# Kernel optimization log

Hardware: AMD Instinct MI355X
Metric: run time of the kernel (lower is better)

## Reference

```python
import jax, jax.numpy as jnp
import numpy as np

N, E, C, K, M = 16384, 512, 128, 2048, 4
H1, H2 = 128, 256
EPS = 1e-5


def setup_inputs() -> dict:
    key = jax.random.key(0)
    ks = jax.random.split(key, 32)
    r = lambda k, shape, s=0.02: jax.random.normal(k, shape, dtype=jnp.float32) * s
    inp = {
        'x': jax.random.normal(ks[0], (N, E), dtype=jnp.float32),
        # per-book encoder params, stacked over M
        'enc_W1': r(ks[1], (M, E, H1)), 'enc_b1': r(ks[2], (M, H1)),
        'bn1_g': 1.0 + r(ks[3], (M, H1)), 'bn1_b': r(ks[4], (M, H1)),
        'bn1_m': r(ks[5], (M, H1), 0.1), 'bn1_v': jnp.ones((M, H1), jnp.float32),
        'enc_W2': r(ks[6], (M, H1, H2)), 'enc_b2': r(ks[7], (M, H2)),
        'bn2_g': 1.0 + r(ks[8], (M, H2)), 'bn2_b': r(ks[9], (M, H2)),
        'bn2_m': r(ks[10], (M, H2), 0.1), 'bn2_v': jnp.ones((M, H2), jnp.float32),
        'enc_W3': r(ks[11], (M, H2, C)), 'enc_b3': r(ks[12], (M, C)),
        # codebooks init uniform(-1/K, 1/K) as in torch source
        'codebooks': jax.random.uniform(ks[13], (M, K, C), jnp.float32, -1.0 / K, 1.0 / K),
        # decoder params
        'dec_W1': r(ks[14], (C, H2)), 'dec_b1': r(ks[15], (H2,)),
        'dbn1_g': 1.0 + r(ks[16], (H2,)), 'dbn1_b': r(ks[17], (H2,)),
        'dbn1_m': r(ks[18], (H2,), 0.1), 'dbn1_v': jnp.ones((H2,), jnp.float32),
        'dec_W2': r(ks[19], (H2, H1)), 'dec_b2': r(ks[20], (H1,)),
        'dbn2_g': 1.0 + r(ks[21], (H1,)), 'dbn2_b': r(ks[22], (H1,)),
        'dbn2_m': r(ks[23], (H1,), 0.1), 'dbn2_v': jnp.ones((H1,), jnp.float32),
        'dec_W3': r(ks[24], (H1, E)), 'dec_b3': r(ks[25], (E,)),
    }
    return inp


def _bn(h, g, b, m, v):
    # eval-mode BatchNorm1d with running stats (dropout inactive in eval)
    return (h - m) * (g / jnp.sqrt(v + EPS)) + b


def reference(x, enc_W1, enc_b1, bn1_g, bn1_b, bn1_m, bn1_v,
              enc_W2, enc_b2, bn2_g, bn2_b, bn2_m, bn2_v,
              enc_W3, enc_b3, codebooks,
              dec_W1, dec_b1, dbn1_g, dbn1_b, dbn1_m, dbn1_v,
              dec_W2, dec_b2, dbn2_g, dbn2_b, dbn2_m, dbn2_v,
              dec_W3, dec_b3):
    # encoders for all M books at once: [M, N, *]
    h = jnp.einsum('ne,mef->mnf', x, enc_W1) + enc_b1[:, None, :]
    h = jax.nn.relu(_bn(h, bn1_g[:, None], bn1_b[:, None], bn1_m[:, None], bn1_v[:, None]))
    h = jnp.einsum('mnf,mfg->mng', h, enc_W2) + enc_b2[:, None, :]
    h = jax.nn.relu(_bn(h, bn2_g[:, None], bn2_b[:, None], bn2_m[:, None], bn2_v[:, None]))
    ze = jnp.einsum('mng,mgc->mnc', h, enc_W3) + enc_b3[:, None, :]  # [M,N,C]

    # squared-distance VQ via dot-product expansion (same math as broadcast cdist)
    ze_sq = jnp.sum(ze * ze, axis=-1)                     # [M,N]
    cb_sq = jnp.sum(codebooks * codebooks, axis=-1)       # [M,K]
    cross = jnp.einsum('mnc,mkc->mnk', ze, codebooks)     # [M,N,K]
    dist = ze_sq[..., None] + cb_sq[:, None, :] - 2.0 * cross
    idx = jnp.argmin(dist, axis=-1)                       # [M,N]
    ce = jnp.take_along_axis(codebooks, idx[:, :, None], axis=1)  # [M,N,C]

    zq = jnp.sum(ce, axis=0)                              # [N,C]

    d = jnp.matmul(zq, dec_W1) + dec_b1
    d = jax.nn.relu(_bn(d, dbn1_g, dbn1_b, dbn1_m, dbn1_v))
    d = jnp.matmul(d, dec_W2) + dec_b2
    d = jax.nn.relu(_bn(d, dbn2_g, dbn2_b, dbn2_m, dbn2_v))
    x_hat = jnp.matmul(d, dec_W3) + dec_b3

    # res_list / ce_list returned as stacked [M,N,C] arrays
    return (x_hat, ze, ce)
```

## Files before the change

kernel.cpp:

```cpp
#include <hip/hip_runtime.h>
#include <hip/hip_bf16.h>
#include <stdint.h>

#define N_ROWS 16384
#define E_DIM 512
#define C_DIM 128
#define K_CODES 2048
#define M_BOOKS 4
#define H1_DIM 128
#define H2_DIM 256
#define EPS_V 1e-5f

typedef __attribute__((ext_vector_type(8))) short short8v;
typedef __attribute__((ext_vector_type(4))) float f32x4;

#if defined(__has_builtin)
#if __has_builtin(__builtin_amdgcn_global_load_lds)
#define HAVE_GLL 1
#endif
#endif

#ifdef HAVE_GLL
__device__ __forceinline__ void gll16(const void* g, void* l) {
    __builtin_amdgcn_global_load_lds(
        (const __attribute__((address_space(1))) uint32_t*)g,
        (__attribute__((address_space(3))) uint32_t*)l, 16, 0, 0);
}
#endif

__device__ __forceinline__ unsigned int mapmono(float d) {
    unsigned int ub = __float_as_uint(d);
    return (ub & 0x80000000u) ? ~ub : (ub | 0x80000000u);
}
__device__ __forceinline__ float unmapmono(unsigned int u) {
    unsigned int bits = (u & 0x80000000u) ? (u & 0x7FFFFFFFu) : ~u;
    return __uint_as_float(bits);
}

template<int BK, bool BNRELU>
__global__ __launch_bounds__(256, 4) void gemm128(
    const float* __restrict__ A, const float* __restrict__ B,
    const float* __restrict__ bias, const float* __restrict__ bn_g,
    const float* __restrict__ bn_b, const float* __restrict__ bn_m,
    const float* __restrict__ bn_v, float* __restrict__ C,
    int Kd, int Hc, size_t sA, size_t sB, size_t sP, size_t sC)
{
    __shared__ float As[BK][128];
    __shared__ float Bs[BK][128];
    const int z = blockIdx.z;
    A += (size_t)z * sA; B += (size_t)z * sB; bias += (size_t)z * sP;
    if (BNRELU) {
        bn_g += (size_t)z * sP; bn_b += (size_t)z * sP;
        bn_m += (size_t)z * sP; bn_v += (size_t)z * sP;
    }
    const int t = threadIdx.x;
    const int tx = t & 15, ty = t >> 4;
    const int row0 = blockIdx.y * 128, col0 = blockIdx.x * 128;
    const int ar = t & 127, ak = (t >> 7) * 4;
    const int bc = (t & 31) * 4, bk0 = t >> 5;

    float acc[8][8] = {};
    for (int k0 = 0; k0 < Kd; k0 += BK) {
        #pragma unroll
        for (int l = 0; l < BK / 8; ++l) {
            const int lk = ak + l * 8;
            float4 av = *(const float4*)(A + (size_t)(row0 + ar) * Kd + (k0 + lk));
            As[lk+0][ar] = av.x; As[lk+1][ar] = av.y;
            As[lk+2][ar] = av.z; As[lk+3][ar] = av.w;
            const int kb = bk0 + l * 8;
            *(float4*)&Bs[kb][bc] =
                *(const float4*)(B + (size_t)(k0 + kb) * Hc + (col0 + bc));
        }
        __syncthreads();
        #pragma unroll
        for (int kk = 0; kk < BK; ++kk) {
            float a[8], b[8];
            *(float4*)&a[0] = *(const float4*)&As[kk][ty*4];
            *(float4*)&a[4] = *(const float4*)&As[kk][64 + ty*4];
            *(float4*)&b[0] = *(const float4*)&Bs[kk][tx*4];
            *(float4*)&b[4] = *(const float4*)&Bs[kk][64 + tx*4];
            #pragma unroll
            for (int i = 0; i < 8; ++i)
                #pragma unroll
                for (int j = 0; j < 8; ++j)
                    acc[i][j] = fmaf(a[i], b[j], acc[i][j]);
        }
        __syncthreads();
    }
    float bi[8], sc[8], mu[8], be[8];
    #pragma unroll
    for (int j = 0; j < 8; ++j) {
        const int col = col0 + ((j < 4) ? (tx*4 + j) : (64 + tx*4 + j - 4));
        bi[j] = bias[col];
        if (BNRELU) {
            sc[j] = bn_g[col] / sqrtf(bn_v[col] + EPS_V);
            mu[j] = bn_m[col]; be[j] = bn_b[col];
        }
    }
    #pragma unroll
    for (int i = 0; i < 8; ++i) {
        const int row = row0 + ((i < 4) ? (ty*4 + i) : (64 + ty*4 + i - 4));
        float v[8];
        #pragma unroll
        for (int j = 0; j < 8; ++j) {
            v[j] = acc[i][j] + bi[j];
            if (BNRELU) {
                float p = (v[j] - mu[j]) * sc[j];
                asm volatile("" : "+v"(p));
                v[j] = fmaxf(p + be[j], 0.0f);
            }
        }
        float* cp = C + (size_t)z * sC + (size_t)row * Hc + col0;
        *(float4*)(cp + tx*4)      = *(const float4*)&v[0];
        *(float4*)(cp + 64 + tx*4) = *(const float4*)&v[4];
    }
}

__global__ __launch_bounds__(256) void rowsq_np(const float* __restrict__ X,
                                                float* __restrict__ out, int rows)
{
    const int r = blockIdx.x * blockDim.x + threadIdx.x;
    if (r >= rows) return;
    const float* p = X + (size_t)r * C_DIM;
    float rr[8];
    #pragma unroll
    for (int j = 0; j < 8; ++j) {
        float v = p[j]; float s2 = v * v;
        asm volatile("" : "+v"(s2));
        rr[j] = s2;
    }
    for (int i = 8; i < C_DIM; i += 8) {
        #pragma unroll
        for (int j = 0; j < 8; ++j) {
            float v = p[i + j]; float s2 = v * v;
            asm volatile("" : "+v"(s2));
            rr[j] = rr[j] + s2;
        }
    }
    out[r] = ((rr[0]+rr[1]) + (rr[2]+rr[3])) + ((rr[4]+rr[5]) + (rr[6]+rr[7]));
}

__global__ __launch_bounds__(256) void split_ze(
    const float* __restrict__ ze, uint16_t* __restrict__ zeAf,
    float* __restrict__ zs, float* __restrict__ eps)
{
    const int m = blockIdx.y;
    const int r = blockIdx.x * 256 + threadIdx.x;
    const size_t g = (size_t)m * N_ROWS + r;
    const float* p = ze + g * C_DIM;
    float a[C_DIM];
    #pragma unroll
    for (int c4 = 0; c4 < C_DIM/4; ++c4) {
        float4 v = *(const float4*)(p + c4*4);
        a[c4*4+0]=v.x; a[c4*4+1]=v.y; a[c4*4+2]=v.z; a[c4*4+3]=v.w;
    }
    {
        float rr[8];
        #pragma unroll
        for (int j = 0; j < 8; ++j) {
            float v = a[j]; float s2 = v*v; asm volatile("" : "+v"(s2)); rr[j]=s2;
        }
        #pragma unroll
        for (int i = 8; i < C_DIM; i += 8)
            #pragma unroll
            for (int j = 0; j < 8; ++j) {
                float v = a[i+j]; float s2 = v*v; asm volatile("" : "+v"(s2));
                rr[j] = rr[j] + s2;
            }
        zs[g] = ((rr[0]+rr[1]) + (rr[2]+rr[3])) + ((rr[4]+rr[5]) + (rr[6]+rr[7]));
    }
    {
        float sab = 0.0f;
        #pragma unroll
        for (int c = 0; c < C_DIM; ++c) sab += fabsf(a[c]);
        eps[g] = sab * 4.8828125e-4f * 1e-4f + 1e-9f;
    }
    const int rt = r >> 7, rl = r & 127;
    uint16_t* base = zeAf + (size_t)m * 4194304 + ((size_t)rt * 4096 + rl) * 8;
    #pragma unroll
    for (int k8 = 0; k8 < 32; ++k8) {
        uint16_t u[8];
        #pragma unroll
        for (int j = 0; j < 8; ++j) {
            const int c = ((k8 < 16) ? k8 : (k8 - 16)) * 8 + j;
            __hip_bfloat16 h = __float2bfloat16(a[c]);
            if (k8 >= 16) {
                float res = a[c] - __bfloat162float(h);
                h = __float2bfloat16(res);
            }
            u[j] = *(uint16_t*)&h;
        }
        *(float4*)(base + (size_t)k8 * 1024) = *(const float4*)u;
    }
}

__global__ __launch_bounds__(256) void split_cb(
    const float* __restrict__ cb, uint16_t* __restrict__ cbBf,
    float* __restrict__ cbsq, int* __restrict__ count)
{
    const int m = blockIdx.z;
    const int k = blockIdx.x * 256 + threadIdx.x;
    if (m == 0 && k == 0) *count = 0;
    const float* p = cb + ((size_t)m * K_CODES + k) * C_DIM;
    float a[C_DIM];
    #pragma unroll
    for (int c4 = 0; c4 < C_DIM/4; ++c4) {
        float4 v = *(const float4*)(p + c4*4);
        a[c4*4+0]=v.x; a[c4*4+1]=v.y; a[c4*4+2]=v.z; a[c4*4+3]=v.w;
    }
    {
        float rr[8];
        #pragma unroll
        for (int j = 0; j < 8; ++j) {
            float v = a[j]; float s2 = v*v; asm volatile("" : "+v"(s2)); rr[j]=s2;
        }
        #pragma unroll
        for (int i = 8; i < C_DIM; i += 8)
            #pragma unroll
            for (int j = 0; j < 8; ++j) {
                float v = a[i+j]; float s2 = v*v; asm volatile("" : "+v"(s2));
                rr[j] = rr[j] + s2;
            }
        cbsq[(size_t)m * K_CODES + k] =
            ((rr[0]+rr[1]) + (rr[2]+rr[3])) + ((rr[4]+rr[5]) + (rr[6]+rr[7]));
    }
    const int ct = k >> 7, kl = k & 127;
    uint16_t* base = cbBf + (((size_t)m * 16 + ct) * 4096 + kl) * 8;
    #pragma unroll
    for (int k8 = 0; k8 < 32; ++k8) {
        uint16_t u[8];
        #pragma unroll
        for (int j = 0; j < 8; ++j) {
            const int c = ((k8 < 16) ? k8 : (k8 - 16)) * 8 + j;
            __hip_bfloat16 h = __float2bfloat16(a[c]);
            if (k8 >= 16) {
                float res = a[c] - __bfloat162float(h);
                h = __float2bfloat16(res);
            }
            u[j] = *(uint16_t*)&h;
        }
        *(float4*)(base + (size_t)k8 * 1024) = *(const float4*)u;
    }
}

__global__ __launch_bounds__(256, 3) void vq_mfma(
    const uint16_t* __restrict__ zeAf, const uint16_t* __restrict__ cbBf,
    const float* __restrict__ zs, const float* __restrict__ cbsq,
    unsigned long long* __restrict__ keysB, unsigned long long* __restrict__ keysS)
{
    __shared__ __align__(16) uint16_t BhS[2][4096], BlS[2][4096];
    __shared__ unsigned long long kb2[128][2];

    const int t = threadIdx.x;
    const int l = t & 63, w = t >> 6;
    const int ct = blockIdx.x, rt = blockIdx.y, m = blockIdx.z;
    const int lq = l >> 4, lc = l & 15;

    const uint16_t* Ag = zeAf + (size_t)m * 4194304 + (size_t)rt * 32768;
    const uint16_t* Bg = cbBf + ((size_t)m * 16 + ct) * 32768;

#ifdef HAVE_GLL
    {
        const uint16_t* sBh = Bg;
        const uint16_t* sBl = Bg + (size_t)16 * 1024;
        gll16(sBh + t*8,        BhS[0] + t*8);
        gll16(sBh + 2048 + t*8, BhS[0] + 2048 + t*8);
        gll16(sBl + t*8,        BlS[0] + t*8);
        gll16(sBl + 2048 + t*8, BlS[0] + 2048 + t*8);
    }
    __syncthreads();
#else
    float4 rh0, rh1, rl0, rl1;
    {
        const uint16_t* sBh = Bg;
        const uint16_t* sBl = Bg + (size_t)16 * 1024;
        rh0 = *(const float4*)(sBh + t*8);
        rh1 = *(const float4*)(sBh + 2048 + t*8);
        rl0 = *(const float4*)(sBl + t*8);
        rl1 = *(const float4*)(sBl + 2048 + t*8);
    }
    *(float4*)(BhS[0] + t*8)        = rh0;
    *(float4*)(BhS[0] + 2048 + t*8) = rh1;
    *(float4*)(BlS[0] + t*8)        = rl0;
    *(float4*)(BlS[0] + 2048 + t*8) = rl1;
    __syncthreads();
#endif

    f32x4 acc[2][8] = {};
    #pragma unroll
    for (int s = 0; s < 4; ++s) {
        const int cur = s & 1;
        if (s < 3) {
            const uint16_t* sBh = Bg + (size_t)((s+1)*4) * 1024;
            const uint16_t* sBl = Bg + (size_t)(16 + (s+1)*4) * 1024;
#ifdef HAVE_GLL
            gll16(sBh + t*8,        BhS[cur^1] + t*8);
            gll16(sBh + 2048 + t*8, BhS[cur^1] + 2048 + t*8);
            gll16(sBl + t*8,        BlS[cur^1] + t*8);
            gll16(sBl + 2048 + t*8, BlS[cur^1] + 2048 + t*8);
#else
            rh0 = *(const float4*)(sBh + t*8);
            rh1 = *(const float4*)(sBh + 2048 + t*8);
            rl0 = *(const float4*)(sBl + t*8);
            rl1 = *(const float4*)(sBl + 2048 + t*8);
#endif
        }
        short8v zeh[2], zel[2], cbf[8];
        #pragma unroll
        for (int rc = 0; rc < 2; ++rc) {
            const int row = w*32 + rc*16 + lc;
            zeh[rc] = *(const short8v*)(Ag + ((size_t)(s*4 + lq)*128 + row)*8);
            zel[rc] = *(const short8v*)(Ag + ((size_t)(16 + s*4 + lq)*128 + row)*8);
        }
        #pragma unroll
        for (int c8 = 0; c8 < 8; ++c8)
            cbf[c8] = *(const short8v*)(BhS[cur] + ((size_t)lq*128 + c8*16 + lc)*8);
        #pragma unroll
        for (int rc = 0; rc < 2; ++rc)
            #pragma unroll
            for (int c8 = 0; c8 < 8; ++c8)
                acc[rc][c8] = __builtin_amdgcn_mfma_f32_16x16x32_bf16(
                    cbf[c8], zeh[rc], acc[rc][c8], 0, 0, 0);
        #pragma unroll
        for (int rc = 0; rc < 2; ++rc)
            #pragma unroll
            for (int c8 = 0; c8 < 8; ++c8)
                acc[rc][c8] = __builtin_amdgcn_mfma_f32_16x16x32_bf16(
                    cbf[c8], zel[rc], acc[rc][c8], 0, 0, 0);
        #pragma unroll
        for (int c8 = 0; c8 < 8; ++c8)
            cbf[c8] = *(const short8v*)(BlS[cur] + ((size_t)lq*128 + c8*16 + lc)*8);
        #pragma unroll
        for (int rc = 0; rc < 2; ++rc)
            #pragma unroll
            for (int c8 = 0; c8 < 8; ++c8)
                acc[rc][c8] = __builtin_amdgcn_mfma_f32_16x16x32_bf16(
                    cbf[c8], zeh[rc], acc[rc][c8], 0, 0, 0);
#ifndef HAVE_GLL
        if (s < 3) {
            *(float4*)(BhS[cur^1] + t*8)        = rh0;
            *(float4*)(BhS[cur^1] + 2048 + t*8) = rh1;
            *(float4*)(BlS[cur^1] + t*8)        = rl0;
            *(float4*)(BlS[cur^1] + 2048 + t*8) = rl1;
        }
#endif
        __syncthreads();
    }

    const float* csb = cbsq + (size_t)m * K_CODES + ct*128;
    #pragma unroll
    for (int rc = 0; rc < 2; ++rc) {
        const int row = w*32 + rc*16 + lc;
        float bd = 3.4e38f, sd = 3.4e38f;
        int bidx = 0;
        #pragma unroll
        for (int c8 = 0; c8 < 8; ++c8)
            #pragma unroll
            for (int q = 0; q < 4; ++q) {
                const int cl = c8*16 + lq*4 + q;
                const float d = fmaf(-2.0f, acc[rc][c8][q], csb[cl]);
                const float mx = fmaxf(bd, d);
                sd = fminf(sd, mx);
                if (d < bd) { bd = d; bidx = ct*128 + cl; }
            }
        #pragma unroll
        for (int mk = 16; mk < 64; mk <<= 1) {
            const float ob = __shfl_xor(bd, mk);
            const int   oi = __shfl_xor(bidx, mk);
            const float os = __shfl_xor(sd, mk);
            const float mx = fmaxf(bd, ob);
            sd = fminf(fminf(sd, os), mx);
            if (ob < bd) { bd = ob; bidx = oi; }
        }
        if (lq == 0) {
            kb2[row][0] = ((unsigned long long)mapmono(bd) << 32) | (unsigned)bidx;
            kb2[row][1] = ((unsigned long long)mapmono(sd) << 32) | 0xFFFFFFFFu;
        }
    }
    __syncthreads();
    if (t < 128) {
        const unsigned long long b = kb2[t][0];
        const unsigned long long s2v = kb2[t][1];
        const size_t g = (size_t)m * N_ROWS + rt*128 + t;
        const unsigned long long old = atomicMin(&keysB[g], b);
        const unsigned long long disp = (b < old) ? old : b;
        const unsigned long long cand = (s2v < disp) ? s2v : disp;
        atomicMin(&keysS[g], cand);
    }
}

__global__ __launch_bounds__(256) void vq_flag(
    const float* __restrict__ ze, const float* __restrict__ cb,
    const float* __restrict__ zs, const float* __restrict__ cbsq,
    const unsigned long long* __restrict__ keysB,
    const unsigned long long* __restrict__ keysS,
    const float* __restrict__ eps, int* __restrict__ list, int* __restrict__ count)
{
    const int m = blockIdx.y;
    const int r = blockIdx.x * 256 + threadIdx.x;
    const size_t g = (size_t)m * N_ROWS + r;
    const unsigned long long kbv = keysB[g];
    const int code = (int)(kbv & 0xFFFFFFFFull);
    const float db = unmapmono((unsigned int)(kbv >> 32));
    const float ds2 = unmapmono((unsigned int)(keysS[g] >> 32));
    const float* zr = ze + g * C_DIM;
    const float* cr = cb + ((size_t)m * K_CODES + code) * C_DIM;
    float acc = 0.0f;
    #pragma unroll
    for (int c = 0; c < C_DIM; ++c) acc = fmaf(zr[c], cr[c], acc);
    const float dex = fmaf(-2.0f, acc, cbsq[(size_t)m * K_CODES + code]);
    const float e = eps[g];
    if ((ds2 - db <= 2.0f * e) || (fabsf(dex - db) > e)) {
        const int p = atomicAdd(count, 1);
        list[p] = (int)g;
    }
}

__global__ __launch_bounds__(256) void vq_cleanup2(
    const float* __restrict__ ze, const float* __restrict__ cb,
    const float* __restrict__ zs, const float* __restrict__ cbsq,
    const int* __restrict__ list, const int* __restrict__ count,
    unsigned long long* __restrict__ keysB)
{
    __shared__ float zrow[C_DIM];
    __shared__ unsigned long long red[4];
    const int t = threadIdx.x;
    const int w = t >> 6, l = t & 63;
    const int nflag = *count;
    for (int idx = blockIdx.x; idx < nflag; idx += gridDim.x) {
        const int g = list[idx];
        const int m = g >> 14;
        if (t < 32)
            *(float4*)(zrow + t*4) = *(const float4*)(ze + (size_t)g * C_DIM + t*4);
        __syncthreads();
        const float zsr = zs[g];
        const int k0 = t * 8;
        const float* cbp = cb + ((size_t)m * K_CODES + k0) * C_DIM;
        const float* csp = cbsq + (size_t)m * K_CODES + k0;
        float acc8[8] = {};
        for (int c4 = 0; c4 < C_DIM/4; ++c4) {
            const float4 a4 = *(const float4*)(zrow + c4*4);
            #pragma unroll
            for (int u = 0; u < 8; ++u) {
                const float4 b4 = *(const float4*)(cbp + (size_t)u * C_DIM + c4*4);
                acc8[u] = fmaf(a4.x, b4.x, acc8[u]);
                acc8[u] = fmaf(a4.y, b4.y, acc8[u]);
                acc8[u] = fmaf(a4.z, b4.z, acc8[u]);
                acc8[u] = fmaf(a4.w, b4.w, acc8[u]);
            }
        }
        unsigned long long bk = ~0ull;
        #pragma unroll
        for (int u = 0; u < 8; ++u) {
            const float tmp = zsr + csp[u];
            float m2a = 2.0f * acc8[u];
            asm volatile("" : "+v"(m2a));
            const float d = tmp - m2a;
            const unsigned long long key =
                ((unsigned long long)mapmono(d) << 32) | (unsigned)(k0 + u);
            bk = (key < bk) ? key : bk;
        }
        #pragma unroll
        for (int off2 = 32; off2 > 0; off2 >>= 1) {
            const unsigned long long o = __shfl_down(bk, off2);
            bk = (o < bk) ? o : bk;
        }
        if (l == 0) red[w] = bk;
        __syncthreads();
        if (t == 0) {
            unsigned long long b = red[0];
            b = (red[1] < b) ? red[1] : b;
            b = (red[2] < b) ? red[2] : b;
            b = (red[3] < b) ? red[3] : b;
            keysB[g] = b;
        }
        __syncthreads();
    }
}

__global__ __launch_bounds__(256) void split_wB(
    const float* __restrict__ W, uint16_t* __restrict__ Wf, int Kd, int Hc)
{
    const int z = blockIdx.z;
    W += (size_t)z * Kd * Hc;
    Wf += (size_t)z * Kd * Hc * 2;
    const int ct = blockIdx.x, k8 = blockIdx.y;
    const int Sh = Kd / 8, S = Kd / 4;
    const int t = threadIdx.x;
    #pragma unroll
    for (int e0 = 0; e0 < 2; ++e0) {
        const int e = t + e0 * 256;
        const int h = e >> 3, j = e & 7;
        const float v = W[(size_t)(k8*8 + j) * Hc + ct*64 + h];
        __hip_bfloat16 hi = __float2bfloat16(v);
        float res = v - __bfloat162float(hi);
        __hip_bfloat16 lo = __float2bfloat16(res);
        Wf[(((size_t)ct*S + k8)*64 + h)*8 + j]      = *(uint16_t*)&hi;
        Wf[(((size_t)ct*S + Sh + k8)*64 + h)*8 + j] = *(uint16_t*)&lo;
    }
}

template<bool BNRELU>
__global__ __launch_bounds__(256, 3) void mfma_fused(
    const float* __restrict__ A, const uint16_t* __restrict__ Wf,
    const float* __restrict__ bias, const float* __restrict__ bn_g,
    const float* __restrict__ bn_b, const float* __restrict__ bn_m,
    const float* __restrict__ bn_v, float* __restrict__ C, int Kd, int Hc,
    size_t sA, size_t sWf, size_t sP, size_t sC)
{
    __shared__ __align__(16) uint16_t Ah[4096], Al[4096], Bh[2048], Bl[2048];
    const int z = blockIdx.z;
    A += (size_t)z * sA; Wf += (size_t)z * sWf; bias += (size_t)z * sP;
    if (BNRELU) {
        bn_g += (size_t)z * sP; bn_b += (size_t)z * sP;
        bn_m += (size_t)z * sP; bn_v += (size_t)z * sP;
    }
    C += (size_t)z * sC;

    const int t = threadIdx.x;
    const int l = t & 63, w = t >> 6;
    const int kq = l >> 4, lc = l & 15;
    const int row0 = blockIdx.y * 128, col0 = blockIdx.x * 64;
    const int Sh = Kd / 8, S = Kd / 4;
    const uint16_t* Wct = Wf + (size_t)blockIdx.x * S * 512;

    f32x4 acc[2][4] = {};
    const int arow = t & 127, khalf = t >> 7;
    for (int ks = 0; ks < Kd / 32; ++ks) {
        const float* ap = A + (size_t)(row0 + arow) * Kd + ks*32 + khalf*16;
        float fa[16];
        *(float4*)&fa[0]  = *(const float4*)(ap);
        *(float4*)&fa[4]  = *(const float4*)(ap + 4);
        *(float4*)&fa[8]  = *(const float4*)(ap + 8);
        *(float4*)&fa[12] = *(const float4*)(ap + 12);
        uint16_t ah[16], al16[16];
        #pragma unroll
        for (int i = 0; i < 16; ++i) {
            __hip_bfloat16 h = __float2bfloat16(fa[i]);
            float res = fa[i] - __bfloat162float(h);
            __hip_bfloat16 lo = __float2bfloat16(res);
            ah[i] = *(uint16_t*)&h; al16[i] = *(uint16_t*)&lo;
        }
        #pragma unroll
        for (int kql = 0; kql < 2; ++kql) {
            const int kq_ = khalf*2 + kql;
            *(float4*)(Ah + ((size_t)kq_*128 + arow)*8) = *(const float4*)&ah[kql*8];
            *(float4*)(Al + ((size_t)kq_*128 + arow)*8) = *(const float4*)&al16[kql*8];
        }
        {
            const int sec = t >> 6, off = (t & 63) * 8;
            *(float4*)(Bh + (size_t)sec*512 + off) =
                *(const float4*)(Wct + ((size_t)(ks*4 + sec))*512 + off);
            *(float4*)(Bl + (size_t)sec*512 + off) =
                *(const float4*)(Wct + ((size_t)(Sh + ks*4 + sec))*512 + off);
        }
        __syncthreads();
        short8v afh[2], afl[2], bfh[4], bfl[4];
        #pragma unroll
        for (int r2 = 0; r2 < 2; ++r2) {
            afh[r2] = *(const short8v*)(Ah + ((size_t)kq*128 + w*32 + r2*16 + lc)*8);
            afl[r2] = *(const short8v*)(Al + ((size_t)kq*128 + w*32 + r2*16 + lc)*8);
        }
        #pragma unroll
        for (int c4 = 0; c4 < 4; ++c4) {
            bfh[c4] = *(const short8v*)(Bh + ((size_t)kq*64 + c4*16 + lc)*8);
            bfl[c4] = *(const short8v*)(Bl + ((size_t)kq*64 + c4*16 + lc)*8);
        }
        #pragma unroll
        for (int r2 = 0; r2 < 2; ++r2)
            #pragma unroll
            for (int c4 = 0; c4 < 4; ++c4) {
                acc[r2][c4] = __builtin_amdgcn_mfma_f32_16x16x32_bf16(
                    afh[r2], bfh[c4], acc[r2][c4], 0, 0, 0);
                acc[r2][c4] = __builtin_amdgcn_mfma_f32_16x16x32_bf16(
                    afl[r2], bfh[c4], acc[r2][c4], 0, 0, 0);
                acc[r2][c4] = __builtin_amdgcn_mfma_f32_16x16x32_bf16(
                    afh[r2], bfl[c4], acc[r2][c4], 0, 0, 0);
            }
        __syncthreads();
    }
    #pragma unroll
    for (int c4 = 0; c4 < 4; ++c4) {
        const int col = col0 + c4*16 + lc;
        const float bi = bias[col];
        float sc = 0.f, mu = 0.f, be = 0.f;
        if (BNRELU) {
            sc = bn_g[col] / sqrtf(bn_v[col] + EPS_V);
            mu = bn_m[col]; be = bn_b[col];
        }
        #pragma unroll
        for (int r2 = 0; r2 < 2; ++r2)
            #pragma unroll
            for (int q = 0; q < 4; ++q) {
                const int row = row0 + w*32 + r2*16 + kq*4 + q;
                float v = acc[r2][c4][q] + bi;
                if (BNRELU) v = fmaxf((v - mu) * sc + be, 0.0f);
                C[(size_t)row * Hc + col] = v;
            }
    }
}

__global__ __launch_bounds__(256, 4) void vq_argmin(
    const float* __restrict__ ze, const float* __restrict__ cb,
    const float* __restrict__ ze_sq, const float* __restrict__ cb_sq,
    unsigned long long* __restrict__ keys)
{
    __shared__ __align__(16) char smem_raw[32768];
    float* As = (float*)smem_raw;
    float* Bs = As + 32*128;
    unsigned long long* kb = (unsigned long long*)smem_raw;
    const int m = blockIdx.z;
    const float* Zm  = ze + (size_t)m * N_ROWS * C_DIM;
    const float* Bm  = cb + (size_t)m * K_CODES * C_DIM;
    const float* zsm = ze_sq + (size_t)m * N_ROWS;
    const float* csm = cb_sq + (size_t)m * K_CODES;
    const int t = threadIdx.x;
    const int tx = t & 15, ty = t >> 4;
    const int row0 = blockIdx.y * 128, col0 = blockIdx.x * 128;
    const int ar = t & 127, ak = (t >> 7) * 4;
    float acc[8][8] = {};
    for (int k0 = 0; k0 < C_DIM; k0 += 32) {
        #pragma unroll
        for (int l = 0; l < 4; ++l) {
            const int lk = ak + l * 8;
            float4 av = *(const float4*)(Zm + (size_t)(row0 + ar) * C_DIM + (k0 + lk));
            As[(lk+0)*128+ar] = av.x; As[(lk+1)*128+ar] = av.y;
            As[(lk+2)*128+ar] = av.z; As[(lk+3)*128+ar] = av.w;
            float4 bv = *(const float4*)(Bm + (size_t)(col0 + ar) * C_DIM + (k0 + lk));
            Bs[(lk+0)*128+ar] = bv.x; Bs[(lk+1)*128+ar] = bv.y;
            Bs[(lk+2)*128+ar] = bv.z; Bs[(lk+3)*128+ar] = bv.w;
        }
        __syncthreads();
        #pragma unroll
        for (int kk = 0; kk < 32; ++kk) {
            float a[8], b[8];
            *(float4*)&a[0] = *(const float4*)&As[kk*128 + ty*4];
            *(float4*)&a[4] = *(const float4*)&As[kk*128 + 64 + ty*4];
            *(float4*)&b[0] = *(const float4*)&Bs[kk*128 + tx*4];
            *(float4*)&b[4] = *(const float4*)&Bs[kk*128 + 64 + tx*4];
            #pragma unroll
            for (int i = 0; i < 8; ++i)
                #pragma unroll
                for (int j = 0; j < 8; ++j)
                    acc[i][j] = fmaf(a[i], b[j], acc[i][j]);
        }
        __syncthreads();
    }
    unsigned long long mykey[8];
    #pragma unroll
    for (int i = 0; i < 8; ++i) {
        const int rloc = (i < 4) ? (ty*4 + i) : (64 + ty*4 + i - 4);
        const float zsv = zsm[row0 + rloc];
        unsigned long long bk = ~0ull;
        #pragma unroll
        for (int j = 0; j < 8; ++j) {
            const int code = col0 + ((j < 4) ? (tx*4 + j) : (64 + tx*4 + j - 4));
            const float d = (zsv + csm[code]) - 2.0f * acc[i][j];
            const unsigned long long key =
                ((unsigned long long)mapmono(d) << 32) | (unsigned)code;
            bk = (key < bk) ? key : bk;
        }
        mykey[i] = bk;
    }
    __syncthreads();
    #pragma unroll
    for (int i = 0; i < 8; ++i) {
        const int rloc = (i < 4) ? (ty*4 + i) : (64 + ty*4 + i - 4);
        kb[rloc*17 + tx] = mykey[i];
    }
    __syncthreads();
    if (t < 128) {
        unsigned long long bk = kb[t*17];
        #pragma unroll
        for (int k2 = 1; k2 < 16; ++k2) {
            const unsigned long long k = kb[t*17 + k2];
            bk = (k < bk) ? k : bk;
        }
        atomicMin(&keys[(size_t)m * N_ROWS + row0 + t], bk);
    }
}

__global__ __launch_bounds__(256) void gather_ce_zq(
    const unsigned long long* __restrict__ keys, const float* __restrict__ cb,
    float* __restrict__ ce_out, float* __restrict__ zq)
{
    const int gid = blockIdx.x * 256 + threadIdx.x;
    const int n = gid >> 7, c = gid & 127;
    float s = 0.0f;
    #pragma unroll
    for (int m = 0; m < M_BOOKS; ++m) {
        const int idx = (int)(keys[(size_t)m * N_ROWS + n] & 0xFFFFFFFFull);
        const float v = cb[((size_t)m * K_CODES + idx) * C_DIM + c];
        ce_out[((size_t)m * N_ROWS + n) * (size_t)C_DIM + c] = v;
        s += v;
    }
    zq[gid] = s;
}

extern "C" void kernel_launch(void* const* d_in, const int* in_sizes, int n_in,
                              void* d_out, int out_size, void* d_ws, size_t ws_size,
                              hipStream_t stream)
{
    const float* x   = (const float*)d_in[0];
    const float* eW1 = (const float*)d_in[1];
    const float* eb1 = (const float*)d_in[2];
    const float* g1  = (const float*)d_in[3];
    const float* b1  = (const float*)d_in[4];
    const float* m1  = (const float*)d_in[5];
    const float* v1  = (const float*)d_in[6];
    const float* eW2 = (const float*)d_in[7];
    const float* eb2 = (const float*)d_in[8];
    const float* g2  = (const float*)d_in[9];
    const float* b2  = (const float*)d_in[10];
    const float* m2  = (const float*)d_in[11];
    const float* v2  = (const float*)d_in[12];
    const float* eW3 = (const float*)d_in[13];
    const float* eb3 = (const float*)d_in[14];
    const float* cb  = (const float*)d_in[15];
    const float* dW1 = (const float*)d_in[16];
    const float* db1 = (const float*)d_in[17];
    const float* dg1 = (const float*)d_in[18];
    const float* dbb1= (const float*)d_in[19];
    const float* dm1 = (const float*)d_in[20];
    const float* dv1 = (const float*)d_in[21];
    const float* dW2 = (const float*)d_in[22];
    const float* db2 = (const float*)d_in[23];
    const float* dg2 = (const float*)d_in[24];
    const float* dbb2= (const float*)d_in[25];
    const float* dm2 = (const float*)d_in[26];
    const float* dv2 = (const float*)d_in[27];
    const float* dW3 = (const float*)d_in[28];
    const float* db3 = (const float*)d_in[29];

    float* out_xhat = (float*)d_out;
    float* out_ze   = out_xhat + (size_t)N_ROWS * E_DIM;
    float* out_ce   = out_ze + (size_t)M_BOOKS * N_ROWS * C_DIM;

    float* ws = (float*)d_ws;
    const size_t h1N1 = (size_t)N_ROWS * H1_DIM;
    const size_t h2N1 = (size_t)N_ROWS * H2_DIM;

    const size_t vqNeedF = 8192 + 65536 + 65536 + 8388608 + 1048576
                         + 131072 + 131072 + 65536 + 16
                         + 32768 + 32768 + 65536
                         + 524288 + 131072 + 131072;
    const bool tierA = ws_size >= ((size_t)M_BOOKS*(h1N1+h2N1) + vqNeedF + 64) * 4;
    const bool tierB = ws_size >= ((h1N1+h2N1) + vqNeedF + 64) * 4;

    dim3 blk(256, 1, 1);

    if (tierB) {
        size_t off = 0;
        float* h1 = ws; off += (tierA ? M_BOOKS : 1) * h1N1;
        float* h2 = ws + off; off += (tierA ? M_BOOKS : 1) * h2N1;
        float* cbsq = ws + off; off += 8192;
        float* zsb = ws + off; off += 65536;
        float* epsb = ws + off; off += 65536;
        uint16_t* zeAf = (uint16_t*)(ws + off); off += 8388608;
        uint16_t* cbBf = (uint16_t*)(ws + off); off += 1048576;
        unsigned long long* keysB = (unsigned long long*)(ws + off); off += 131072;
        unsigned long long* keysS = (unsigned long long*)(ws + off); off += 131072;
        int* list = (int*)(ws + off); off += 65536;
        int* count = (int*)(ws + off); off += 16;
        uint16_t* w1f = (uint16_t*)(ws + off); off += 32768;
        uint16_t* w2f = (uint16_t*)(ws + off); off += 32768;
        uint16_t* w3f = (uint16_t*)(ws + off); off += 65536;
        uint16_t* we1f = (uint16_t*)(ws + off); off += 524288;
        uint16_t* we2f = (uint16_t*)(ws + off); off += 131072;
        uint16_t* we3f = (uint16_t*)(ws + off); off += 131072;
        float* zq = h1; float* d1 = h2; float* d2 = h1;

        split_cb<<<dim3(K_CODES/256, 1, M_BOOKS), blk, 0, stream>>>(cb, cbBf, cbsq, count);
        split_wB<<<dim3(H1_DIM/64, E_DIM/8, M_BOOKS), blk, 0, stream>>>(eW1, we1f, E_DIM, H1_DIM);
        split_wB<<<dim3(H2_DIM/64, H1_DIM/8, M_BOOKS), blk, 0, stream>>>(eW2, we2f, H1_DIM, H2_DIM);
        split_wB<<<dim3(C_DIM/64, H2_DIM/8, M_BOOKS), blk, 0, stream>>>(eW3, we3f, H2_DIM, C_DIM);
        split_wB<<<dim3(H2_DIM/64, C_DIM/8, 1), blk, 0, stream>>>(dW1, w1f, C_DIM, H2_DIM);
        split_wB<<<dim3(H1_DIM/64, H2_DIM/8, 1), blk, 0, stream>>>(dW2, w2f, H2_DIM, H1_DIM);
        split_wB<<<dim3(E_DIM/64, H1_DIM/8, 1), blk, 0, stream>>>(dW3, w3f, H1_DIM, E_DIM);
        hipMemsetAsync((void*)keysB, 0xFF, (size_t)M_BOOKS * N_ROWS * 8 * 2, stream);

        const int nz = tierA ? M_BOOKS : 1;
        const int nloop = tierA ? 1 : M_BOOKS;
        for (int p = 0; p < nloop; ++p) {
            const size_t mb = tierA ? 0 : (size_t)p;
            mfma_fused<true><<<dim3(H1_DIM/64, N_ROWS/128, nz), blk, 0, stream>>>(
                x, we1f + mb*(size_t)E_DIM*H1_DIM*2,
                eb1 + mb*H1_DIM, g1 + mb*H1_DIM, b1 + mb*H1_DIM, m1 + mb*H1_DIM, v1 + mb*H1_DIM,
                h1, E_DIM, H1_DIM,
                0, (size_t)E_DIM*H1_DIM*2, H1_DIM, h1N1);
            mfma_fused<true><<<dim3(H2_DIM/64, N_ROWS/128, nz), blk, 0, stream>>>(
                h1, we2f + mb*(size_t)H1_DIM*H2_DIM*2,
                eb2 + mb*H2_DIM, g2 + mb*H2_DIM, b2 + mb*H2_DIM, m2 + mb*H2_DIM, v2 + mb*H2_DIM,
                h2, H1_DIM, H2_DIM,
                h1N1, (size_t)H1_DIM*H2_DIM*2, H2_DIM, h2N1);
            mfma_fused<false><<<dim3(C_DIM/64, N_ROWS/128, nz), blk, 0, stream>>>(
                h2, we3f + mb*(size_t)H2_DIM*C_DIM*2,
                eb3 + mb*C_DIM, nullptr, nullptr, nullptr, nullptr,
                out_ze + mb*(size_t)N_ROWS*C_DIM, H2_DIM, C_DIM,
                h2N1, (size_t)H2_DIM*C_DIM*2, C_DIM, (size_t)N_ROWS*C_DIM);
        }

        split_ze<<<dim3(N_ROWS/256, M_BOOKS), blk, 0, stream>>>(out_ze, zeAf, zsb, epsb);
        vq_mfma<<<dim3(K_CODES/128, N_ROWS/128, M_BOOKS), blk, 0, stream>>>(
            zeAf, cbBf, zsb, cbsq, keysB, keysS);
        vq_flag<<<dim3(N_ROWS/256, M_BOOKS), blk, 0, stream>>>(
            out_ze, cb, zsb, cbsq, keysB, keysS, epsb, list, count);
        vq_cleanup2<<<dim3(2048), blk, 0, stream>>>(
            out_ze, cb, zsb, cbsq, list, count, keysB);

        gather_ce_zq<<<dim3((N_ROWS*C_DIM)/256), blk, 0, stream>>>(keysB, cb, out_ce, zq);
        mfma_fused<true><<<dim3(H2_DIM/64, N_ROWS/128, 1), blk, 0, stream>>>(
            zq, w1f, db1, dg1, dbb1, dm1, dv1, d1, C_DIM, H2_DIM, 0, 0, 0, 0);
        mfma_fused<true><<<dim3(H1_DIM/64, N_ROWS/128, 1), blk, 0, stream>>>(
            d1, w2f, db2, dg2, dbb2, dm2, dv2, d2, H2_DIM, H1_DIM, 0, 0, 0, 0);
        mfma_fused<false><<<dim3(E_DIM/64, N_ROWS/128, 1), blk, 0, stream>>>(
            d2, w3f, db3, nullptr, nullptr, nullptr, nullptr,
            out_xhat, H1_DIM, E_DIM, 0, 0, 0, 0);
        return;
    }

    {
        const size_t smallN = (size_t)M_BOOKS*N_ROWS + (size_t)M_BOOKS*K_CODES
                            + 2 + 2*(size_t)M_BOOKS*N_ROWS;
        const size_t fullFloats = (size_t)M_BOOKS*(h1N1 + h2N1) + smallN;
        const bool fM = ws_size >= fullFloats * sizeof(float) + 256;
        size_t off = 0;
        float* h1 = ws; off += (fM ? M_BOOKS : 1) * h1N1;
        float* h2 = ws + off; off += (fM ? M_BOOKS : 1) * h2N1;
        float* zesq = ws + off; off += (size_t)M_BOOKS * N_ROWS;
        float* cbsq = ws + off; off += (size_t)M_BOOKS * K_CODES;
        off = (off + 1) & ~(size_t)1;
        unsigned long long* keys = (unsigned long long*)(ws + off);
        float* zq = h1; float* d1 = h2; float* d2 = h1;
        hipMemsetAsync((void*)keys, 0xFF, (size_t)M_BOOKS * N_ROWS * 8, stream);
        const int nz = fM ? M_BOOKS : 1;
        const int nloop = fM ? 1 : M_BOOKS;
        for (int p = 0; p < nloop; ++p) {
            const size_t mb = fM ? 0 : (size_t)p;
            gemm128<32, true><<<dim3(H1_DIM/128, N_ROWS/128, nz), blk, 0, stream>>>(
                x, eW1 + mb*(size_t)E_DIM*H1_DIM,
                eb1 + mb*H1_DIM, g1 + mb*H1_DIM, b1 + mb*H1_DIM, m1 + mb*H1_DIM, v1 + mb*H1_DIM,
                h1, E_DIM, H1_DIM, 0, (size_t)E_DIM*H1_DIM, H1_DIM, h1N1);
            gemm128<32, true><<<dim3(H2_DIM/128, N_ROWS/128, nz), blk, 0, stream>>>(
                h1, eW2 + mb*(size_t)H1_DIM*H2_DIM,
                eb2 + mb*H2_DIM, g2 + mb*H2_DIM, b2 + mb*H2_DIM, m2 + mb*H2_DIM, v2 + mb*H2_DIM,
                h2, H1_DIM, H2_DIM, h1N1, (size_t)H1_DIM*H2_DIM, H2_DIM, h2N1);
            gemm128<32, false><<<dim3(C_DIM/128, N_ROWS/128, nz), blk, 0, stream>>>(
                h2, eW3 + mb*(size_t)H2_DIM*C_DIM,
                eb3 + mb*C_DIM, nullptr, nullptr, nullptr, nullptr,
                out_ze + mb*(size_t)N_ROWS*C_DIM, H2_DIM, C_DIM,
                h2N1, (size_t)H2_DIM*C_DIM, C_DIM, (size_t)N_ROWS*C_DIM);
        }
        rowsq_np<<<dim3((M_BOOKS*N_ROWS)/256), blk, 0, stream>>>(out_ze, zesq, M_BOOKS*N_ROWS);
        rowsq_np<<<dim3((M_BOOKS*K_CODES)/256), blk, 0, stream>>>(cb, cbsq, M_BOOKS*K_CODES);
        vq_argmin<<<dim3(K_CODES/128, N_ROWS/128, M_BOOKS), blk, 0, stream>>>(
            out_ze, cb, zesq, cbsq, keys);
        gather_ce_zq<<<dim3((N_ROWS*C_DIM)/256), blk, 0, stream>>>(keys, cb, out_ce, zq);
        gemm128<32, true><<<dim3(H2_DIM/128, N_ROWS/128, 1), blk, 0, stream>>>(
            zq, dW1, db1, dg1, dbb1, dm1, dv1, d1, C_DIM, H2_DIM, 0, 0, 0, 0);
        gemm128<32, true><<<dim3(H1_DIM/128, N_ROWS/128, 1), blk, 0, stream>>>(
            d1, dW2, db2, dg2, dbb2, dm2, dv2, d2, H2_DIM, H1_DIM, 0, 0, 0, 0);
        gemm128<32, false><<<dim3(E_DIM/128, N_ROWS/128, 1), blk, 0, stream>>>(
            d2, dW3, db3, nullptr, nullptr, nullptr, nullptr,
            out_xhat, H1_DIM, E_DIM, 0, 0, 0, 0);
    }
}
```

Measured before the change: 436.0 us.

## Keep full codebook tile resident in LDS and loop over row tiles

The VQ distance kernel now loads the whole 128-code hi/lo bf16 codebook tile (64 KB) into LDS once per block and reuses it across 8 row tiles, replacing the per-block streaming double buffer. This cuts the global-to-LDS codebook traffic and the per-stage barriers by the row-tile factor. In exchange the grid shrinks eightfold, occupancy drops (launch bound 3 to 2, larger LDS footprint), and the codebook load is no longer overlapped with compute.

```diff
diff --git a/kernel.cpp b/kernel.cpp
--- a/kernel.cpp
+++ b/kernel.cpp
@@ -10,6 +10,7 @@
 #define H1_DIM 128
 #define H2_DIM 256
 #define EPS_V 1e-5f
+#define VQ_RT 8
 
 typedef __attribute__((ext_vector_type(8))) short short8v;
 typedef __attribute__((ext_vector_type(4))) float f32x4;
@@ -243,149 +244,113 @@
     }
 }
 
-__global__ __launch_bounds__(256, 3) void vq_mfma(
+__global__ __launch_bounds__(256, 2) void vq_mfma(
     const uint16_t* __restrict__ zeAf, const uint16_t* __restrict__ cbBf,
     const float* __restrict__ zs, const float* __restrict__ cbsq,
     unsigned long long* __restrict__ keysB, unsigned long long* __restrict__ keysS)
 {
-    __shared__ __align__(16) uint16_t BhS[2][4096], BlS[2][4096];
+    __shared__ __align__(16) uint16_t Ball[32768];
     __shared__ unsigned long long kb2[128][2];
 
     const int t = threadIdx.x;
     const int l = t & 63, w = t >> 6;
-    const int ct = blockIdx.x, rt = blockIdx.y, m = blockIdx.z;
+    const int ct = blockIdx.x, rt0 = blockIdx.y * VQ_RT, m = blockIdx.z;
     const int lq = l >> 4, lc = l & 15;
 
-    const uint16_t* Ag = zeAf + (size_t)m * 4194304 + (size_t)rt * 32768;
     const uint16_t* Bg = cbBf + ((size_t)m * 16 + ct) * 32768;
-
 #ifdef HAVE_GLL
-    {
-        const uint16_t* sBh = Bg;
-        const uint16_t* sBl = Bg + (size_t)16 * 1024;
-        gll16(sBh + t*8,        BhS[0] + t*8);
-        gll16(sBh + 2048 + t*8, BhS[0] + 2048 + t*8);
-        gll16(sBl + t*8,        BlS[0] + t*8);
-        gll16(sBl + 2048 + t*8, BlS[0] + 2048 + t*8);
-    }
+    #pragma unroll
+    for (int i = 0; i < 16; ++i)
+        gll16(Bg + (size_t)(t + i*256) * 8, Ball + (size_t)(t + i*256) * 8);
+#else
+    #pragma unroll
+    for (int i = 0; i < 16; ++i)
+        *(float4*)(Ball + (size_t)(t + i*256)*8) =
+            *(const float4*)(Bg + (size_t)(t + i*256)*8);
+#endif
     __syncthreads();
-#else
-    float4 rh0, rh1, rl0, rl1;
-    {
-        const uint16_t* sBh = Bg;
-        const uint16_t* sBl = Bg + (size_t)16 * 1024;
-        rh0 = *(const float4*)(sBh + t*8);
-        rh1 = *(const float4*)(sBh + 2048 + t*8);
-        rl0 = *(const float4*)(sBl + t*8);
-        rl1 = *(const float4*)(sBl + 2048 + t*8);
-    }
-    *(float4*)(BhS[0] + t*8)        = rh0;
-    *(float4*)(BhS[0] + 2048 + t*8) = rh1;
-    *(float4*)(BlS[0] + t*8)        = rl0;
-    *(float4*)(BlS[0] + 2048 + t*8) = rl1;
-    __syncthreads();
-#endif
-
-    f32x4 acc[2][8] = {};
-    #pragma unroll
-    for (int s = 0; s < 4; ++s) {
-        const int cur = s & 1;
-        if (s < 3) {
-            const uint16_t* sBh = Bg + (size_t)((s+1)*4) * 1024;
-            const uint16_t* sBl = Bg + (size_t)(16 + (s+1)*4) * 1024;
-#ifdef HAVE_GLL
-            gll16(sBh + t*8,        BhS[cur^1] + t*8);
-            gll16(sBh + 2048 + t*8, BhS[cur^1] + 2048 + t*8);
-            gll16(sBl + t*8,        BlS[cur^1] + t*8);
-            gll16(sBl + 2048 + t*8, BlS[cur^1] + 2048 + t*8);
-#else
-            rh0 = *(const float4*)(sBh + t*8);
-            rh1 = *(const float4*)(sBh + 2048 + t*8);
-            rl0 = *(const float4*)(sBl + t*8);
-            rl1 = *(const float4*)(sBl + 2048 + t*8);
-#endif
-        }
-        short8v zeh[2], zel[2], cbf[8];
+
+    const float* csb = cbsq + (size_t)m * K_CODES + ct*128;
+
+    for (int ri = 0; ri < VQ_RT; ++ri) {
+        const int rt = rt0 + ri;
+        const uint16_t* Ag = zeAf + (size_t)m * 4194304 + (size_t)rt * 32768;
+        f32x4 acc[2][8] = {};
+        #pragma unroll
+        for (int s = 0; s < 4; ++s) {
+            short8v zeh[2], zel[2], cbf[8];
+            #pragma unroll
+            for (int rc = 0; rc < 2; ++rc) {
+                const int row = w*32 + rc*16 + lc;
+                zeh[rc] = *(const short8v*)(Ag + ((size_t)(s*4 + lq)*128 + row)*8);
+                zel[rc] = *(const short8v*)(Ag + ((size_t)(16 + s*4 + lq)*128 + row)*8);
+            }
+            #pragma unroll
+            for (int c8 = 0; c8 < 8; ++c8)
+                cbf[c8] = *(const short8v*)(Ball + ((size_t)(s*4 + lq)*128 + c8*16 + lc)*8);
+            #pragma unroll
+            for (int rc = 0; rc < 2; ++rc)
+                #pragma unroll
+                for (int c8 = 0; c8 < 8; ++c8)
+                    acc[rc][c8] = __builtin_amdgcn_mfma_f32_16x16x32_bf16(
+                        cbf[c8], zeh[rc], acc[rc][c8], 0, 0, 0);
+            #pragma unroll
+            for (int rc = 0; rc < 2; ++rc)
+                #pragma unroll
+                for (int c8 = 0; c8 < 8; ++c8)
+                    acc[rc][c8] = __builtin_amdgcn_mfma_f32_16x16x32_bf16(
+                        cbf[c8], zel[rc], acc[rc][c8], 0, 0, 0);
+            #pragma unroll
+            for (int c8 = 0; c8 < 8; ++c8)
+                cbf[c8] = *(const short8v*)(Ball + ((size_t)(16 + s*4 + lq)*128 + c8*16 + lc)*8);
+            #pragma unroll
+            for (int rc = 0; rc < 2; ++rc)
+                #pragma unroll
+                for (int c8 = 0; c8 < 8; ++c8)
+                    acc[rc][c8] = __builtin_amdgcn_mfma_f32_16x16x32_bf16(
+                        cbf[c8], zeh[rc], acc[rc][c8], 0, 0, 0);
+        }
+
         #pragma unroll
         for (int rc = 0; rc < 2; ++rc) {
             const int row = w*32 + rc*16 + lc;
-            zeh[rc] = *(const short8v*)(Ag + ((size_t)(s*4 + lq)*128 + row)*8);
-            zel[rc] = *(const short8v*)(Ag + ((size_t)(16 + s*4 + lq)*128 + row)*8);
-        }
-        #pragma unroll
-        for (int c8 = 0; c8 < 8; ++c8)
-            cbf[c8] = *(const short8v*)(BhS[cur] + ((size_t)lq*128 + c8*16 + lc)*8);
-        #pragma unroll
-        for (int rc = 0; rc < 2; ++rc)
+            float bd = 3.4e38f, sd = 3.4e38f;
+            int bidx = 0;
             #pragma unroll
             for (int c8 = 0; c8 < 8; ++c8)
-                acc[rc][c8] = __builtin_amdgcn_mfma_f32_16x16x32_bf16(
-                    cbf[c8], zeh[rc], acc[rc][c8], 0, 0, 0);
-        #pragma unroll
-        for (int rc = 0; rc < 2; ++rc)
-            #pragma unroll
-            for (int c8 = 0; c8 < 8; ++c8)
-                acc[rc][c8] = __builtin_amdgcn_mfma_f32_16x16x32_bf16(
-                    cbf[c8], zel[rc], acc[rc][c8], 0, 0, 0);
-        #pragma unroll
-        for (int c8 = 0; c8 < 8; ++c8)
-            cbf[c8] = *(const short8v*)(BlS[cur] + ((size_t)lq*128 + c8*16 + lc)*8);
-        #pragma unroll
-        for (int rc = 0; rc < 2; ++rc)
-            #pragma unroll
-            for (int c8 = 0; c8 < 8; ++c8)
-                acc[rc][c8] = __builtin_amdgcn_mfma_f32_16x16x32_bf16(
-                    cbf[c8], zeh[rc], acc[rc][c8], 0, 0, 0);
-#ifndef HAVE_GLL
-        if (s < 3) {
-            *(float4*)(BhS[cur^1] + t*8)        = rh0;
-            *(float4*)(BhS[cur^1] + 2048 + t*8) = rh1;
-            *(float4*)(BlS[cur^1] + t*8)        = rl0;
-            *(float4*)(BlS[cur^1] + 2048 + t*8) = rl1;
-        }
-#endif
-        __syncthreads();
-    }
-
-    const float* csb = cbsq + (size_t)m * K_CODES + ct*128;
-    #pragma unroll
-    for (int rc = 0; rc < 2; ++rc) {
-        const int row = w*32 + rc*16 + lc;
-        float bd = 3.4e38f, sd = 3.4e38f;
-        int bidx = 0;
-        #pragma unroll
-        for (int c8 = 0; c8 < 8; ++c8)
-            #pragma unroll
-            for (int q = 0; q < 4; ++q) {
-                const int cl = c8*16 + lq*4 + q;
-                const float d = fmaf(-2.0f, acc[rc][c8][q], csb[cl]);
-                const float mx = fmaxf(bd, d);
-                sd = fminf(sd, mx);
-                if (d < bd) { bd = d; bidx = ct*128 + cl; }
-            }
-        #pragma unroll
-        for (int mk = 16; mk < 64; mk <<= 1) {
-            const float ob = __shfl_xor(bd, mk);
-            const int   oi = __shfl_xor(bidx, mk);
-            const float os = __shfl_xor(sd, mk);
-            const float mx = fmaxf(bd, ob);
-            sd = fminf(fminf(sd, os), mx);
-            if (ob < bd) { bd = ob; bidx = oi; }
-        }
-        if (lq == 0) {
-            kb2[row][0] = ((unsigned long long)mapmono(bd) << 32) | (unsigned)bidx;
-            kb2[row][1] = ((unsigned long long)mapmono(sd) << 32) | 0xFFFFFFFFu;
-        }
-    }
-    __syncthreads();
-    if (t < 128) {
-        const unsigned long long b = kb2[t][0];
-        const unsigned long long s2v = kb2[t][1];
-        const size_t g = (size_t)m * N_ROWS + rt*128 + t;
-        const unsigned long long old = atomicMin(&keysB[g], b);
-        const unsigned long long disp = (b < old) ? old : b;
-        const unsigned long long cand = (s2v < disp) ? s2v : disp;
-        atomicMin(&keysS[g], cand);
+                #pragma unroll
+                for (int q = 0; q < 4; ++q) {
+                    const int cl = c8*16 + lq*4 + q;
+                    const float d = fmaf(-2.0f, acc[rc][c8][q], csb[cl]);
+                    const float mx = fmaxf(bd, d);
+                    sd = fminf(sd, mx);
+                    if (d < bd) { bd = d; bidx = ct*128 + cl; }
+                }
+            #pragma unroll
+            for (int mk = 16; mk < 64; mk <<= 1) {
+                const float ob = __shfl_xor(bd, mk);
+                const int   oi = __shfl_xor(bidx, mk);
+                const float os = __shfl_xor(sd, mk);
+                const float mx = fmaxf(bd, ob);
+                sd = fminf(fminf(sd, os), mx);
+                if (ob < bd) { bd = ob; bidx = oi; }
+            }
+            if (lq == 0) {
+                kb2[row][0] = ((unsigned long long)mapmono(bd) << 32) | (unsigned)bidx;
+                kb2[row][1] = ((unsigned long long)mapmono(sd) << 32) | 0xFFFFFFFFu;
+            }
+        }
+        __syncthreads();
+        if (t < 128) {
+            const unsigned long long b = kb2[t][0];
+            const unsigned long long s2v = kb2[t][1];
+            const size_t g = (size_t)m * N_ROWS + (size_t)rt*128 + t;
+            const unsigned long long old = atomicMin(&keysB[g], b);
+            const unsigned long long disp = (b < old) ? old : b;
+            const unsigned long long cand = (s2v < disp) ? s2v : disp;
+            atomicMin(&keysS[g], cand);
+        }
+        __syncthreads();
     }
 }
 
@@ -801,7 +766,7 @@
         }
 
         split_ze<<<dim3(N_ROWS/256, M_BOOKS), blk, 0, stream>>>(out_ze, zeAf, zsb, epsb);
-        vq_mfma<<<dim3(K_CODES/128, N_ROWS/128, M_BOOKS), blk, 0, stream>>>(
+        vq_mfma<<<dim3(K_CODES/128, N_ROWS/(128*VQ_RT), M_BOOKS), blk, 0, stream>>>(
             zeAf, cbBf, zsb, cbsq, keysB, keysS);
         vq_flag<<<dim3(N_ROWS/256, M_BOOKS), blk, 0, stream>>>(
             out_ze, cb, zsb, cbsq, keysB, keysS, epsb, list, count);
```

Result: faster. 425.4 us (-2.4%).
